# Performance work log

Measured on AMD Instinct MI355X. Metric: run time of the kernel, lower is better.

The kernel has to match this reference:

```python
import jax, jax.numpy as jnp
import numpy as np

T, B, H = 128, 256, 1024


def setup_inputs() -> dict:
    key = jax.random.key(0)
    ks = jax.random.split(key, 6)
    s_i = 1.0 / np.sqrt(2 * H)   # lecun-ish scale for input kernel [2H,3H]
    s_h = 1.0 / np.sqrt(H)       # recurrent kernel scale
    return {
        "a_target": jax.random.normal(ks[0], (T, B, H), jnp.float32),
        "resets": jax.random.bernoulli(ks[1], 0.05, (T, B)),
        "W_i": jax.random.normal(ks[2], (2 * H, 3 * H), jnp.float32) * s_i,
        "b_i": jnp.zeros((3 * H,), jnp.float32),
        "W_h": jax.random.normal(ks[3], (H, 3 * H), jnp.float32) * s_h,
        "b_hn": jnp.zeros((H,), jnp.float32),
        "W_p": jax.random.normal(ks[4], (H, H), jnp.float32) * np.sqrt(2.0 / H),
        "b_p": jnp.zeros((H,), jnp.float32),
    }


def reference(a_target, resets, W_i, b_i, W_h, b_hn, W_p, b_p):
    Hd = W_h.shape[0]
    Bn = a_target.shape[1]

    def step(carry, xt):
        h, a_hat = carry
        a_t, rst = xt                     # a_t: [B,H], rst: [B] bool
        m = rst[:, None]
        h = jnp.where(m, 0.0, h)          # reset-masking of carry
        a_hat = jnp.where(m, 0.0, a_hat)
        pos = jax.nn.relu(a_t - a_hat)
        neg = jax.nn.relu(a_hat - a_t)
        e_t = jnp.concatenate([pos, neg], axis=-1)          # [B, 2H]
        err_mag = jnp.mean(pos + neg, axis=-1)              # [B]
        # GRUCell: gates r,z,n (flax convention: bias on input path + candidate h path)
        gi = e_t @ W_i + b_i                                # [B, 3H]
        gh = h @ W_h                                        # [B, 3H]
        i_r, i_z, i_n = jnp.split(gi, 3, axis=-1)
        h_r, h_z, h_n = jnp.split(gh, 3, axis=-1)
        r = jax.nn.sigmoid(i_r + h_r)
        z = jax.nn.sigmoid(i_z + h_z)
        n = jnp.tanh(i_n + r * (h_n + b_hn))
        new_h = (1.0 - z) * n + z * h                       # [B, H]
        new_a_hat = jax.nn.relu(new_h @ W_p + b_p)          # prediction_dense + relu
        return (new_h, new_a_hat), (new_h, err_mag)

    init = (jnp.zeros((Bn, Hd), a_target.dtype),
            jnp.zeros((Bn, Hd), a_target.dtype))
    (_, _), (r_ts, err_mags) = jax.lax.scan(step, init, (a_target, resets))
    return r_ts, err_mags  # [T,B,H], [T,B]
```

## Files before the change

### kernel.cpp

```cpp
#include <hip/hip_runtime.h>
#include <hip/hip_bf16.h>
#include <math.h>

#define T_DIM 128
#define B_DIM 256
#define H_DIM 1024
#define N3    3072
#define KC    3072
#define KTC   96
#define KTP   32

typedef __attribute__((ext_vector_type(8))) short short8;
typedef __attribute__((ext_vector_type(4))) float float4v;
typedef __attribute__((ext_vector_type(4))) unsigned short ushort4v;

__device__ __forceinline__ unsigned short f2bf(float f) {
  union { float f; unsigned u; } v; v.f = f;
  unsigned u = v.u;
  unsigned r = u + 0x7FFFu + ((u >> 16) & 1u);
  return (unsigned short)(r >> 16);
}

__device__ __forceinline__ size_t afrag(int m, int k, int KT) {
  return ((((size_t)(m >> 4) * KT) + (k >> 5)) * 64
          + ((((k >> 3) & 3) << 4) | (m & 15))) * 8 + (k & 7);
}

__device__ __forceinline__ void store_bf4(unsigned short* p, const float* v) {
  ushort4v u;
  u.x = f2bf(v[0]); u.y = f2bf(v[1]); u.z = f2bf(v[2]); u.w = f2bf(v[3]);
  *(ushort4v*)p = u;
}

__device__ __forceinline__ float sigm(float x) { return 1.f / (1.f + __expf(-x)); }

__global__ void detect_resets(const int* __restrict__ r, int* __restrict__ flag) {
  __shared__ int f;
  if (threadIdx.x == 0) f = 0;
  __syncthreads();
  int loc = 0;
  for (int i = threadIdx.x; i < 8192; i += 256) {
    if ((unsigned)r[i] > 1u) loc = 1;
  }
  if (loc) f = 1;
  __syncthreads();
  if (threadIdx.x == 0) *flag = f;
}

__global__ __launch_bounds__(256) void decode_resets(
    const void* __restrict__ resets, const int* __restrict__ rflag,
    unsigned char* __restrict__ rb) {
  int t = blockIdx.x, b = threadIdx.x;
  int v;
  if (*rflag) v = (int)((const unsigned char*)resets)[t * B_DIM + b];
  else        v = ((const int*)resets)[t * B_DIM + b];
  rb[t * B_DIM + b] = (v != 0) ? 1 : 0;
}

__global__ __launch_bounds__(256) void convert_gates(
    const float* __restrict__ Wi, const float* __restrict__ Wh,
    unsigned short* __restrict__ Wg) {
  int nt = blockIdx.x;
  int kt = blockIdx.y;
  int jt = nt >> 2, g = nt & 3;
  size_t base = ((size_t)nt * KTC + kt) * 512;
  for (int e = threadIdx.x; e < 512; e += 256) {
    int i = e & 7, l = (e >> 3) & 63;
    int k = (kt << 5) + ((l >> 4) << 3) + i;
    int j = (jt << 4) + (l & 15);
    float v = 0.f;
    if (g == 0) v = (k < 2048) ? Wi[(size_t)k * N3 + j] : Wh[(size_t)(k - 2048) * N3 + j];
    else if (g == 1) v = (k < 2048) ? Wi[(size_t)k * N3 + 1024 + j] : Wh[(size_t)(k - 2048) * N3 + 1024 + j];
    else if (g == 2) { if (k < 2048) v = Wi[(size_t)k * N3 + 2048 + j]; }
    else             { if (k >= 2048) v = Wh[(size_t)(k - 2048) * N3 + 2048 + j]; }
    Wg[base + e] = f2bf(v);
  }
}

__global__ __launch_bounds__(256) void convert_wp(const float* __restrict__ W,
                                                  unsigned short* __restrict__ Wsw) {
  int nt = blockIdx.x;
  int kt = blockIdx.y;
  size_t base = ((size_t)nt * KTP + kt) * 512;
  for (int e = threadIdx.x; e < 512; e += 256) {
    int i = e & 7, l = (e >> 3) & 63;
    int k = (kt << 5) + ((l >> 4) << 3) + i;
    int n = (nt << 4) + (l & 15);
    Wsw[base + e] = f2bf(W[(size_t)k * H_DIM + n]);
  }
}

__global__ __launch_bounds__(256) void init_state(
    const float* __restrict__ a_all,
    unsigned short* __restrict__ A0, float* __restrict__ h0,
    float* __restrict__ err_out) {
  int b = blockIdx.x, tid = threadIdx.x;
  int j0 = tid * 4;
  const float* arow = a_all + (size_t)b * H_DIM;
  float pv[4], nv[4], zz[4] = {0.f, 0.f, 0.f, 0.f};
  float s = 0.f;
#pragma unroll
  for (int jj = 0; jj < 4; ++jj) {
    float a = arow[j0 + jj];
    pv[jj] = fmaxf(a, 0.f);
    nv[jj] = fmaxf(-a, 0.f);
    s += pv[jj] + nv[jj];
    h0[(size_t)b * H_DIM + j0 + jj] = 0.f;
  }
  store_bf4(A0 + afrag(b, j0, KTC), pv);
  store_bf4(A0 + afrag(b, 1024 + j0, KTC), nv);
  store_bf4(A0 + afrag(b, 2048 + j0, KTC), zz);
  __shared__ float red[256];
  red[tid] = s;
  __syncthreads();
  for (int st = 128; st > 0; st >>= 1) {
    if (tid < st) red[tid] += red[tid + st];
    __syncthreads();
  }
  if (tid == 0) err_out[b] = red[0] * (1.0f / (float)H_DIM);
}

__device__ __forceinline__ void load_chunk4(
    const short8* __restrict__ ap0, const short8* __restrict__ ap1,
    const short8* __restrict__ ap2, const short8* __restrict__ ap3,
    const short8* __restrict__ bpr, const short8* __restrict__ bpz,
    const short8* __restrict__ bpn, int kb,
    short8 (&A)[4][2], short8 (&R)[2], short8 (&Z)[2], short8 (&N)[2]) {
  size_t o0 = (size_t)kb * 64, o1 = (size_t)(kb + 1) * 64;
  A[0][0] = ap0[o0]; A[1][0] = ap1[o0]; A[2][0] = ap2[o0]; A[3][0] = ap3[o0];
  A[0][1] = ap0[o1]; A[1][1] = ap1[o1]; A[2][1] = ap2[o1]; A[3][1] = ap3[o1];
  R[0] = bpr[o0]; Z[0] = bpz[o0]; N[0] = bpn[o0];
  R[1] = bpr[o1]; Z[1] = bpz[o1]; N[1] = bpn[o1];
}

template<int GS>
__device__ __forceinline__ void mfma_chunk4(
    float4v (&acc)[4][4],
    const short8 (&A)[4][2], const short8 (&R)[2], const short8 (&Z)[2],
    const short8 (&N)[2]) {
#pragma unroll
  for (int kk = 0; kk < 2; ++kk) {
#pragma unroll
    for (int mi = 0; mi < 4; ++mi) {
      acc[mi][0]  = __builtin_amdgcn_mfma_f32_16x16x32_bf16(A[mi][kk], R[kk], acc[mi][0], 0, 0, 0);
      acc[mi][1]  = __builtin_amdgcn_mfma_f32_16x16x32_bf16(A[mi][kk], Z[kk], acc[mi][1], 0, 0, 0);
      acc[mi][GS] = __builtin_amdgcn_mfma_f32_16x16x32_bf16(A[mi][kk], N[kk], acc[mi][GS], 0, 0, 0);
    }
  }
}

template<int GS>
__device__ __forceinline__ void gates_seg4(
    float4v (&acc)[4][4],
    const short8* __restrict__ ap0, const short8* __restrict__ ap1,
    const short8* __restrict__ ap2, const short8* __restrict__ ap3,
    const short8* __restrict__ bpr, const short8* __restrict__ bpz,
    const short8* __restrict__ bpn, int kbeg, int kend) {
  if (kbeg >= kend) return;
  short8 Aa[4][2], Ra[2], Za[2], Na[2];
  short8 Ab[4][2], Rb[2], Zb[2], Nb[2];
  load_chunk4(ap0, ap1, ap2, ap3, bpr, bpz, bpn, kbeg, Aa, Ra, Za, Na);
  for (int kb = kbeg; kb < kend; kb += 4) {
    load_chunk4(ap0, ap1, ap2, ap3, bpr, bpz, bpn, kb + 2, Ab, Rb, Zb, Nb);
    mfma_chunk4<GS>(acc, Aa, Ra, Za, Na);
    if (kb + 4 < kend)
      load_chunk4(ap0, ap1, ap2, ap3, bpr, bpz, bpn, kb + 4, Aa, Ra, Za, Na);
    mfma_chunk4<GS>(acc, Ab, Rb, Zb, Nb);
  }
}

__global__ __launch_bounds__(512, 2) void gates_fused(
    const unsigned short* __restrict__ A_sw, const unsigned short* __restrict__ Wg,
    const float* __restrict__ b_i, const float* __restrict__ b_hn,
    const float* __restrict__ h_in, float* __restrict__ h_out,
    unsigned short* __restrict__ A_next,
    const unsigned char* __restrict__ rb,
    float* __restrict__ r_out, int t) {
  int lane = threadIdx.x & 63, wave = threadIdx.x >> 6;
  int b = blockIdx.x;
  int jt = b & 63;
  int rg2 = b >> 6;

  __shared__ float4v red[4][4][2][64];

  const short8* A8 = (const short8*)A_sw;
  const short8* B8 = (const short8*)Wg;

  float4v acc[4][4];
#pragma unroll
  for (int mi = 0; mi < 4; ++mi)
#pragma unroll
    for (int g = 0; g < 4; ++g) acc[mi][g] = (float4v){0.f, 0.f, 0.f, 0.f};

  const short8* ap0 = A8 + ((size_t)(rg2 * 4 + 0) * KTC) * 64 + lane;
  const short8* ap1 = A8 + ((size_t)(rg2 * 4 + 1) * KTC) * 64 + lane;
  const short8* ap2 = A8 + ((size_t)(rg2 * 4 + 2) * KTC) * 64 + lane;
  const short8* ap3 = A8 + ((size_t)(rg2 * 4 + 3) * KTC) * 64 + lane;
  const short8* bpr = B8 + ((size_t)(jt * 4 + 0) * KTC) * 64 + lane;
  const short8* bpz = B8 + ((size_t)(jt * 4 + 1) * KTC) * 64 + lane;
  const short8* bpi = B8 + ((size_t)(jt * 4 + 2) * KTC) * 64 + lane;
  const short8* bph = B8 + ((size_t)(jt * 4 + 3) * KTC) * 64 + lane;

  int k0 = wave * 12, k1 = k0 + 12;
  int e_end = (k1 < 64) ? k1 : 64;
  int h_st  = (k0 > 64) ? k0 : 64;

  gates_seg4<2>(acc, ap0, ap1, ap2, ap3, bpr, bpz, bpi, k0, e_end);
  gates_seg4<3>(acc, ap0, ap1, ap2, ap3, bpr, bpz, bph, h_st, k1);

#pragma unroll
  for (int hh = 0; hh < 2; ++hh) {
    if (wave >= 4) {
#pragma unroll
      for (int mi = 0; mi < 4; ++mi) {
        red[wave - 4][mi][0][lane] = acc[mi][2 * hh];
        red[wave - 4][mi][1][lane] = acc[mi][2 * hh + 1];
      }
    }
    __syncthreads();
    if (wave < 4) {
#pragma unroll
      for (int mi = 0; mi < 4; ++mi) {
        acc[mi][2 * hh]     += red[wave][mi][0][lane];
        acc[mi][2 * hh + 1] += red[wave][mi][1][lane];
      }
    }
    __syncthreads();
  }
  float4v accs[4];
#pragma unroll
  for (int hh = 0; hh < 2; ++hh) {
    if (wave < 4) {
#pragma unroll
      for (int mi = 0; mi < 4; ++mi) {
        red[wave][mi][0][lane] = acc[mi][2 * hh];
        red[wave][mi][1][lane] = acc[mi][2 * hh + 1];
      }
    }
    __syncthreads();
    if (wave < 4) {
      float4v s0 = red[0][wave][0][lane];
      float4v s1 = red[0][wave][1][lane];
#pragma unroll
      for (int w = 1; w < 4; ++w) {
        s0 += red[w][wave][0][lane];
        s1 += red[w][wave][1][lane];
      }
      accs[2 * hh] = s0; accs[2 * hh + 1] = s1;
    }
    __syncthreads();
  }

  if (wave < 4) {
    int cl = lane & 15, q = lane >> 4;
    int jcol = (jt << 4) + cl;
    float br_ = b_i[jcol], bz_ = b_i[1024 + jcol], bn_ = b_i[2048 + jcol];
    float bh = b_hn[jcol];
    int row_base = rg2 * 64 + wave * 16 + q * 4;
#pragma unroll
    for (int rr = 0; rr < 4; ++rr) {
      int row = row_base + rr;
      float r = sigm(accs[0][rr] + br_);
      float z = sigm(accs[1][rr] + bz_);
      float n = tanhf(accs[2][rr] + bn_ + r * (accs[3][rr] + bh));
      float hv = h_in[(size_t)row * H_DIM + jcol];
      float nh = (1.f - z) * n + z * hv;
      r_out[((size_t)t * B_DIM + row) * H_DIM + jcol] = nh;
      if (t < T_DIM - 1) {
        int rst = rb[(t + 1) * B_DIM + row];
        float hm = rst ? 0.f : nh;
        h_out[(size_t)row * H_DIM + jcol] = hm;
        A_next[afrag(row, 2048 + jcol, KTC)] = f2bf(hm);
      }
    }
  }
}

__global__ __launch_bounds__(512, 2) void pred_fused(
    const unsigned short* __restrict__ A_next, const unsigned short* __restrict__ Wp,
    const float* __restrict__ b_p, const float* __restrict__ a_all,
    const unsigned char* __restrict__ rb,
    unsigned short* __restrict__ A_next_w, float* __restrict__ err_out, int t) {
  int lane = threadIdx.x & 63, wave = threadIdx.x >> 6;
  int b = blockIdx.x;
  int ntq = b & 15, mt = b >> 4;

  const short8* A8 = (const short8*)A_next;
  const short8* B8 = (const short8*)Wp;

  const short8* hap = A8 + ((size_t)mt * KTC + 64) * 64 + lane;
  const short8* bp0 = B8 + ((size_t)(ntq * 4 + 0) * KTP) * 64 + lane;
  const short8* bp1 = B8 + ((size_t)(ntq * 4 + 1) * KTP) * 64 + lane;
  const short8* bp2 = B8 + ((size_t)(ntq * 4 + 2) * KTP) * 64 + lane;
  const short8* bp3 = B8 + ((size_t)(ntq * 4 + 3) * KTP) * 64 + lane;

  float4v acc[4];
#pragma unroll
  for (int n = 0; n < 4; ++n) acc[n] = (float4v){0.f, 0.f, 0.f, 0.f};

  {
    int pk0 = wave * 4;
    short8 Aa[4], B0a[4], B1a[4], B2a[4], B3a[4];
#pragma unroll
    for (int kk = 0; kk < 4; ++kk) Aa[kk] = hap[(size_t)(pk0 + kk) * 64];
#pragma unroll
    for (int kk = 0; kk < 4; ++kk) {
      size_t o = (size_t)(pk0 + kk) * 64;
      B0a[kk] = bp0[o]; B1a[kk] = bp1[o]; B2a[kk] = bp2[o]; B3a[kk] = bp3[o];
    }
#pragma unroll
    for (int kk = 0; kk < 4; ++kk) {
      acc[0] = __builtin_amdgcn_mfma_f32_16x16x32_bf16(Aa[kk], B0a[kk], acc[0], 0, 0, 0);
      acc[1] = __builtin_amdgcn_mfma_f32_16x16x32_bf16(Aa[kk], B1a[kk], acc[1], 0, 0, 0);
      acc[2] = __builtin_amdgcn_mfma_f32_16x16x32_bf16(Aa[kk], B2a[kk], acc[2], 0, 0, 0);
      acc[3] = __builtin_amdgcn_mfma_f32_16x16x32_bf16(Aa[kk], B3a[kk], acc[3], 0, 0, 0);
    }
  }

  __shared__ float4v red[8][4][64];
  __shared__ float rsum_red[4][4][4];
#pragma unroll
  for (int n = 0; n < 4; ++n) red[wave][n][lane] = acc[n];
  __syncthreads();

  int cl = lane & 15, q = lane >> 4;

  if (wave < 4) {
    float4v s = red[0][wave][lane];
#pragma unroll
    for (int w = 1; w < 8; ++w) s += red[w][wave][lane];

    int coln = (ntq * 4 + wave) * 16 + cl;
    float bp = b_p[coln];
    float rsum[4];
#pragma unroll
    for (int rr = 0; rr < 4; ++rr) {
      int row = mt * 16 + q * 4 + rr;
      float ah = fmaxf(s[rr] + bp, 0.f);
      int rst = rb[(t + 1) * B_DIM + row];
      float am = rst ? 0.f : ah;
      float av = a_all[((size_t)(t + 1) * B_DIM + row) * H_DIM + coln];
      float d = av - am;
      float pos = fmaxf(d, 0.f), neg = fmaxf(-d, 0.f);
      A_next_w[afrag(row, coln, KTC)] = f2bf(pos);
      A_next_w[afrag(row, 1024 + coln, KTC)] = f2bf(neg);
      rsum[rr] = pos + neg;
    }
#pragma unroll
    for (int rr = 0; rr < 4; ++rr) {
      float sv = rsum[rr];
      sv += __shfl_xor(sv, 1);
      sv += __shfl_xor(sv, 2);
      sv += __shfl_xor(sv, 4);
      sv += __shfl_xor(sv, 8);
      if (cl == 0) rsum_red[wave][q][rr] = sv;
    }
  }
  __syncthreads();
  if (wave == 0 && lane < 16) {
    int qq = lane >> 2, rr = lane & 3;
    float sv = rsum_red[0][qq][rr] + rsum_red[1][qq][rr]
             + rsum_red[2][qq][rr] + rsum_red[3][qq][rr];
    int row = mt * 16 + qq * 4 + rr;
    atomicAdd(err_out + (size_t)(t + 1) * B_DIM + row, sv * (1.0f / (float)H_DIM));
  }
}

extern "C" void kernel_launch(void* const* d_in, const int* in_sizes, int n_in,
                              void* d_out, int out_size, void* d_ws, size_t ws_size,
                              hipStream_t stream) {
  (void)in_sizes; (void)n_in; (void)out_size; (void)ws_size;
  const float* a_all = (const float*)d_in[0];
  const void*  resets = d_in[1];
  const float* W_i  = (const float*)d_in[2];
  const float* b_i  = (const float*)d_in[3];
  const float* W_h  = (const float*)d_in[4];
  const float* b_hn = (const float*)d_in[5];
  const float* W_p  = (const float*)d_in[6];
  const float* b_p  = (const float*)d_in[7];

  float* r_out = (float*)d_out;
  float* err_out = r_out + (size_t)T_DIM * B_DIM * H_DIM;

  char* ws = (char*)d_ws;
  unsigned short* Wg_sw = (unsigned short*)ws; ws += (size_t)256 * 16 * KC * 2;
  unsigned short* Wp_sw = (unsigned short*)ws; ws += (size_t)H_DIM * H_DIM * 2;
  unsigned short* A0    = (unsigned short*)ws; ws += (size_t)B_DIM * KC * 2;
  unsigned short* A1    = (unsigned short*)ws; ws += (size_t)B_DIM * KC * 2;
  float* h0 = (float*)ws; ws += (size_t)B_DIM * H_DIM * 4;
  float* h1 = (float*)ws; ws += (size_t)B_DIM * H_DIM * 4;
  unsigned char* rb = (unsigned char*)ws; ws += T_DIM * B_DIM;
  int* rflag = (int*)ws; ws += 256;

  hipMemsetAsync(err_out, 0, (size_t)T_DIM * B_DIM * sizeof(float), stream);
  detect_resets<<<1, 256, 0, stream>>>((const int*)resets, rflag);
  decode_resets<<<T_DIM, 256, 0, stream>>>(resets, rflag, rb);
  convert_gates<<<dim3(256, KTC), 256, 0, stream>>>(W_i, W_h, Wg_sw);
  convert_wp<<<dim3(H_DIM / 16, KTP), 256, 0, stream>>>(W_p, Wp_sw);
  init_state<<<B_DIM, 256, 0, stream>>>(a_all, A0, h0, err_out);

  for (int t = 0; t < T_DIM; ++t) {
    const unsigned short* Acur = (t & 1) ? A1 : A0;
    unsigned short* Anext      = (t & 1) ? A0 : A1;
    const float* hcur = (t & 1) ? h1 : h0;
    float* hnext      = (t & 1) ? h0 : h1;
    gates_fused<<<256, 512, 0, stream>>>(
        Acur, Wg_sw, b_i, b_hn, hcur, hnext, Anext, rb, r_out, t);
    if (t < T_DIM - 1)
      pred_fused<<<256, 512, 0, stream>>>(
          Anext, Wp_sw, b_p, a_all, rb, Anext, err_out, t);
  }
}
```

Baseline: 2.502 ms.

## Split gates kernel rows across two wave groups with 1024-thread blocks

```diff
diff --git a/kernel.cpp b/kernel.cpp
--- a/kernel.cpp
+++ b/kernel.cpp
@@ -120,28 +120,27 @@
   if (tid == 0) err_out[b] = red[0] * (1.0f / (float)H_DIM);
 }
 
-__device__ __forceinline__ void load_chunk4(
+__device__ __forceinline__ void load_chunk2(
     const short8* __restrict__ ap0, const short8* __restrict__ ap1,
-    const short8* __restrict__ ap2, const short8* __restrict__ ap3,
     const short8* __restrict__ bpr, const short8* __restrict__ bpz,
     const short8* __restrict__ bpn, int kb,
-    short8 (&A)[4][2], short8 (&R)[2], short8 (&Z)[2], short8 (&N)[2]) {
+    short8 (&A)[2][2], short8 (&R)[2], short8 (&Z)[2], short8 (&N)[2]) {
   size_t o0 = (size_t)kb * 64, o1 = (size_t)(kb + 1) * 64;
-  A[0][0] = ap0[o0]; A[1][0] = ap1[o0]; A[2][0] = ap2[o0]; A[3][0] = ap3[o0];
-  A[0][1] = ap0[o1]; A[1][1] = ap1[o1]; A[2][1] = ap2[o1]; A[3][1] = ap3[o1];
+  A[0][0] = ap0[o0]; A[1][0] = ap1[o0];
+  A[0][1] = ap0[o1]; A[1][1] = ap1[o1];
   R[0] = bpr[o0]; Z[0] = bpz[o0]; N[0] = bpn[o0];
   R[1] = bpr[o1]; Z[1] = bpz[o1]; N[1] = bpn[o1];
 }
 
 template<int GS>
-__device__ __forceinline__ void mfma_chunk4(
-    float4v (&acc)[4][4],
-    const short8 (&A)[4][2], const short8 (&R)[2], const short8 (&Z)[2],
+__device__ __forceinline__ void mfma_chunk2(
+    float4v (&acc)[2][4],
+    const short8 (&A)[2][2], const short8 (&R)[2], const short8 (&Z)[2],
     const short8 (&N)[2]) {
 #pragma unroll
   for (int kk = 0; kk < 2; ++kk) {
 #pragma unroll
-    for (int mi = 0; mi < 4; ++mi) {
+    for (int mi = 0; mi < 2; ++mi) {
       acc[mi][0]  = __builtin_amdgcn_mfma_f32_16x16x32_bf16(A[mi][kk], R[kk], acc[mi][0], 0, 0, 0);
       acc[mi][1]  = __builtin_amdgcn_mfma_f32_16x16x32_bf16(A[mi][kk], Z[kk], acc[mi][1], 0, 0, 0);
       acc[mi][GS] = __builtin_amdgcn_mfma_f32_16x16x32_bf16(A[mi][kk], N[kk], acc[mi][GS], 0, 0, 0);
@@ -150,26 +149,25 @@
 }
 
 template<int GS>
-__device__ __forceinline__ void gates_seg4(
-    float4v (&acc)[4][4],
+__device__ __forceinline__ void gates_seg2(
+    float4v (&acc)[2][4],
     const short8* __restrict__ ap0, const short8* __restrict__ ap1,
-    const short8* __restrict__ ap2, const short8* __restrict__ ap3,
     const short8* __restrict__ bpr, const short8* __restrict__ bpz,
     const short8* __restrict__ bpn, int kbeg, int kend) {
   if (kbeg >= kend) return;
-  short8 Aa[4][2], Ra[2], Za[2], Na[2];
-  short8 Ab[4][2], Rb[2], Zb[2], Nb[2];
-  load_chunk4(ap0, ap1, ap2, ap3, bpr, bpz, bpn, kbeg, Aa, Ra, Za, Na);
+  short8 Aa[2][2], Ra[2], Za[2], Na[2];
+  short8 Ab[2][2], Rb[2], Zb[2], Nb[2];
+  load_chunk2(ap0, ap1, bpr, bpz, bpn, kbeg, Aa, Ra, Za, Na);
   for (int kb = kbeg; kb < kend; kb += 4) {
-    load_chunk4(ap0, ap1, ap2, ap3, bpr, bpz, bpn, kb + 2, Ab, Rb, Zb, Nb);
-    mfma_chunk4<GS>(acc, Aa, Ra, Za, Na);
+    load_chunk2(ap0, ap1, bpr, bpz, bpn, kb + 2, Ab, Rb, Zb, Nb);
+    mfma_chunk2<GS>(acc, Aa, Ra, Za, Na);
     if (kb + 4 < kend)
-      load_chunk4(ap0, ap1, ap2, ap3, bpr, bpz, bpn, kb + 4, Aa, Ra, Za, Na);
-    mfma_chunk4<GS>(acc, Ab, Rb, Zb, Nb);
-  }
-}
-
-__global__ __launch_bounds__(512, 2) void gates_fused(
+      load_chunk2(ap0, ap1, bpr, bpz, bpn, kb + 4, Aa, Ra, Za, Na);
+    mfma_chunk2<GS>(acc, Ab, Rb, Zb, Nb);
+  }
+}
+
+__global__ __launch_bounds__(1024, 1) void gates_fused(
     const unsigned short* __restrict__ A_sw, const unsigned short* __restrict__ Wg,
     const float* __restrict__ b_i, const float* __restrict__ b_hn,
     const float* __restrict__ h_in, float* __restrict__ h_out,
@@ -177,52 +175,52 @@
     const unsigned char* __restrict__ rb,
     float* __restrict__ r_out, int t) {
   int lane = threadIdx.x & 63, wave = threadIdx.x >> 6;
+  int mg = wave >> 3;
+  int ks = wave & 7;
   int b = blockIdx.x;
   int jt = b & 63;
   int rg2 = b >> 6;
 
-  __shared__ float4v red[4][4][2][64];
+  __shared__ float4v red[2][4][2][2][64];
 
   const short8* A8 = (const short8*)A_sw;
   const short8* B8 = (const short8*)Wg;
 
-  float4v acc[4][4];
-#pragma unroll
-  for (int mi = 0; mi < 4; ++mi)
+  float4v acc[2][4];
+#pragma unroll
+  for (int mi = 0; mi < 2; ++mi)
 #pragma unroll
     for (int g = 0; g < 4; ++g) acc[mi][g] = (float4v){0.f, 0.f, 0.f, 0.f};
 
-  const short8* ap0 = A8 + ((size_t)(rg2 * 4 + 0) * KTC) * 64 + lane;
-  const short8* ap1 = A8 + ((size_t)(rg2 * 4 + 1) * KTC) * 64 + lane;
-  const short8* ap2 = A8 + ((size_t)(rg2 * 4 + 2) * KTC) * 64 + lane;
-  const short8* ap3 = A8 + ((size_t)(rg2 * 4 + 3) * KTC) * 64 + lane;
+  const short8* ap0 = A8 + ((size_t)(rg2 * 4 + mg * 2 + 0) * KTC) * 64 + lane;
+  const short8* ap1 = A8 + ((size_t)(rg2 * 4 + mg * 2 + 1) * KTC) * 64 + lane;
   const short8* bpr = B8 + ((size_t)(jt * 4 + 0) * KTC) * 64 + lane;
   const short8* bpz = B8 + ((size_t)(jt * 4 + 1) * KTC) * 64 + lane;
   const short8* bpi = B8 + ((size_t)(jt * 4 + 2) * KTC) * 64 + lane;
   const short8* bph = B8 + ((size_t)(jt * 4 + 3) * KTC) * 64 + lane;
 
-  int k0 = wave * 12, k1 = k0 + 12;
+  int k0 = ks * 12, k1 = k0 + 12;
   int e_end = (k1 < 64) ? k1 : 64;
   int h_st  = (k0 > 64) ? k0 : 64;
 
-  gates_seg4<2>(acc, ap0, ap1, ap2, ap3, bpr, bpz, bpi, k0, e_end);
-  gates_seg4<3>(acc, ap0, ap1, ap2, ap3, bpr, bpz, bph, h_st, k1);
+  gates_seg2<2>(acc, ap0, ap1, bpr, bpz, bpi, k0, e_end);
+  gates_seg2<3>(acc, ap0, ap1, bpr, bpz, bph, h_st, k1);
 
 #pragma unroll
   for (int hh = 0; hh < 2; ++hh) {
-    if (wave >= 4) {
-#pragma unroll
-      for (int mi = 0; mi < 4; ++mi) {
-        red[wave - 4][mi][0][lane] = acc[mi][2 * hh];
-        red[wave - 4][mi][1][lane] = acc[mi][2 * hh + 1];
+    if (ks >= 4) {
+#pragma unroll
+      for (int mi = 0; mi < 2; ++mi) {
+        red[mg][ks - 4][mi][0][lane] = acc[mi][2 * hh];
+        red[mg][ks - 4][mi][1][lane] = acc[mi][2 * hh + 1];
       }
     }
     __syncthreads();
-    if (wave < 4) {
-#pragma unroll
-      for (int mi = 0; mi < 4; ++mi) {
-        acc[mi][2 * hh]     += red[wave][mi][0][lane];
-        acc[mi][2 * hh + 1] += red[wave][mi][1][lane];
+    if (ks < 4) {
+#pragma unroll
+      for (int mi = 0; mi < 2; ++mi) {
+        acc[mi][2 * hh]     += red[mg][ks][mi][0][lane];
+        acc[mi][2 * hh + 1] += red[mg][ks][mi][1][lane];
       }
     }
     __syncthreads();
@@ -230,33 +228,33 @@
   float4v accs[4];
 #pragma unroll
   for (int hh = 0; hh < 2; ++hh) {
-    if (wave < 4) {
-#pragma unroll
-      for (int mi = 0; mi < 4; ++mi) {
-        red[wave][mi][0][lane] = acc[mi][2 * hh];
-        red[wave][mi][1][lane] = acc[mi][2 * hh + 1];
+    if (ks < 4) {
+#pragma unroll
+      for (int mi = 0; mi < 2; ++mi) {
+        red[mg][ks][mi][0][lane] = acc[mi][2 * hh];
+        red[mg][ks][mi][1][lane] = acc[mi][2 * hh + 1];
       }
     }
     __syncthreads();
-    if (wave < 4) {
-      float4v s0 = red[0][wave][0][lane];
-      float4v s1 = red[0][wave][1][lane];
+    if (ks < 2) {
+      float4v s0 = red[mg][0][ks][0][lane];
+      float4v s1 = red[mg][0][ks][1][lane];
 #pragma unroll
       for (int w = 1; w < 4; ++w) {
-        s0 += red[w][wave][0][lane];
-        s1 += red[w][wave][1][lane];
+        s0 += red[mg][w][ks][0][lane];
+        s1 += red[mg][w][ks][1][lane];
       }
       accs[2 * hh] = s0; accs[2 * hh + 1] = s1;
     }
     __syncthreads();
   }
 
-  if (wave < 4) {
+  if (ks < 2) {
     int cl = lane & 15, q = lane >> 4;
     int jcol = (jt << 4) + cl;
     float br_ = b_i[jcol], bz_ = b_i[1024 + jcol], bn_ = b_i[2048 + jcol];
     float bh = b_hn[jcol];
-    int row_base = rg2 * 64 + wave * 16 + q * 4;
+    int row_base = rg2 * 64 + (mg * 2 + ks) * 16 + q * 4;
 #pragma unroll
     for (int rr = 0; rr < 4; ++rr) {
       int row = row_base + rr;
@@ -404,7 +402,7 @@
     unsigned short* Anext      = (t & 1) ? A0 : A1;
     const float* hcur = (t & 1) ? h1 : h0;
     float* hnext      = (t & 1) ? h0 : h1;
-    gates_fused<<<256, 512, 0, stream>>>(
+    gates_fused<<<256, 1024, 0, stream>>>(
         Acur, Wg_sw, b_i, b_hn, hcur, hnext, Anext, rb, r_out, t);
     if (t < T_DIM - 1)
       pred_fused<<<256, 512, 0, stream>>>(
```

Measured after the change: 3.235 ms. +29.3%, slower.

## Stage gate GEMM operands through LDS with async global_load_lds double buffering

Applied to the files above, without the earlier changes.

```diff
diff --git a/kernel.cpp b/kernel.cpp
--- a/kernel.cpp
+++ b/kernel.cpp
@@ -33,6 +33,12 @@
 }
 
 __device__ __forceinline__ float sigm(float x) { return 1.f / (1.f + __expf(-x)); }
+
+__device__ __forceinline__ void glds16(const void* gsrc, void* ldst) {
+  __builtin_amdgcn_global_load_lds(
+      (const __attribute__((address_space(1))) unsigned int*)gsrc,
+      (__attribute__((address_space(3))) unsigned int*)ldst, 16, 0, 0);
+}
 
 __global__ void detect_resets(const int* __restrict__ r, int* __restrict__ flag) {
   __shared__ int f;
@@ -120,56 +126,7 @@
   if (tid == 0) err_out[b] = red[0] * (1.0f / (float)H_DIM);
 }
 
-__device__ __forceinline__ void load_chunk4(
-    const short8* __restrict__ ap0, const short8* __restrict__ ap1,
-    const short8* __restrict__ ap2, const short8* __restrict__ ap3,
-    const short8* __restrict__ bpr, const short8* __restrict__ bpz,
-    const short8* __restrict__ bpn, int kb,
-    short8 (&A)[4][2], short8 (&R)[2], short8 (&Z)[2], short8 (&N)[2]) {
-  size_t o0 = (size_t)kb * 64, o1 = (size_t)(kb + 1) * 64;
-  A[0][0] = ap0[o0]; A[1][0] = ap1[o0]; A[2][0] = ap2[o0]; A[3][0] = ap3[o0];
-  A[0][1] = ap0[o1]; A[1][1] = ap1[o1]; A[2][1] = ap2[o1]; A[3][1] = ap3[o1];
-  R[0] = bpr[o0]; Z[0] = bpz[o0]; N[0] = bpn[o0];
-  R[1] = bpr[o1]; Z[1] = bpz[o1]; N[1] = bpn[o1];
-}
-
-template<int GS>
-__device__ __forceinline__ void mfma_chunk4(
-    float4v (&acc)[4][4],
-    const short8 (&A)[4][2], const short8 (&R)[2], const short8 (&Z)[2],
-    const short8 (&N)[2]) {
-#pragma unroll
-  for (int kk = 0; kk < 2; ++kk) {
-#pragma unroll
-    for (int mi = 0; mi < 4; ++mi) {
-      acc[mi][0]  = __builtin_amdgcn_mfma_f32_16x16x32_bf16(A[mi][kk], R[kk], acc[mi][0], 0, 0, 0);
-      acc[mi][1]  = __builtin_amdgcn_mfma_f32_16x16x32_bf16(A[mi][kk], Z[kk], acc[mi][1], 0, 0, 0);
-      acc[mi][GS] = __builtin_amdgcn_mfma_f32_16x16x32_bf16(A[mi][kk], N[kk], acc[mi][GS], 0, 0, 0);
-    }
-  }
-}
-
-template<int GS>
-__device__ __forceinline__ void gates_seg4(
-    float4v (&acc)[4][4],
-    const short8* __restrict__ ap0, const short8* __restrict__ ap1,
-    const short8* __restrict__ ap2, const short8* __restrict__ ap3,
-    const short8* __restrict__ bpr, const short8* __restrict__ bpz,
-    const short8* __restrict__ bpn, int kbeg, int kend) {
-  if (kbeg >= kend) return;
-  short8 Aa[4][2], Ra[2], Za[2], Na[2];
-  short8 Ab[4][2], Rb[2], Zb[2], Nb[2];
-  load_chunk4(ap0, ap1, ap2, ap3, bpr, bpz, bpn, kbeg, Aa, Ra, Za, Na);
-  for (int kb = kbeg; kb < kend; kb += 4) {
-    load_chunk4(ap0, ap1, ap2, ap3, bpr, bpz, bpn, kb + 2, Ab, Rb, Zb, Nb);
-    mfma_chunk4<GS>(acc, Aa, Ra, Za, Na);
-    if (kb + 4 < kend)
-      load_chunk4(ap0, ap1, ap2, ap3, bpr, bpz, bpn, kb + 4, Aa, Ra, Za, Na);
-    mfma_chunk4<GS>(acc, Ab, Rb, Zb, Nb);
-  }
-}
-
-__global__ __launch_bounds__(512, 2) void gates_fused(
+__global__ __launch_bounds__(512, 1) void gates_fused(
     const unsigned short* __restrict__ A_sw, const unsigned short* __restrict__ Wg,
     const float* __restrict__ b_i, const float* __restrict__ b_hn,
     const float* __restrict__ h_in, float* __restrict__ h_out,
@@ -181,32 +138,81 @@
   int jt = b & 63;
   int rg2 = b >> 6;
 
-  __shared__ float4v red[4][4][2][64];
+  __shared__ short8 stage[2][8][7][64];
 
   const short8* A8 = (const short8*)A_sw;
   const short8* B8 = (const short8*)Wg;
 
+  const short8* aB0 = A8 + ((size_t)(rg2 * 4 + 0) * KTC) * 64;
+  const short8* aB1 = A8 + ((size_t)(rg2 * 4 + 1) * KTC) * 64;
+  const short8* aB2 = A8 + ((size_t)(rg2 * 4 + 2) * KTC) * 64;
+  const short8* aB3 = A8 + ((size_t)(rg2 * 4 + 3) * KTC) * 64;
+  const short8* wBr = B8 + ((size_t)(jt * 4 + 0) * KTC) * 64;
+  const short8* wBz = B8 + ((size_t)(jt * 4 + 1) * KTC) * 64;
+  const short8* wBi = B8 + ((size_t)(jt * 4 + 2) * KTC) * 64;
+  const short8* wBh = B8 + ((size_t)(jt * 4 + 3) * KTC) * 64;
+
   float4v acc[4][4];
 #pragma unroll
   for (int mi = 0; mi < 4; ++mi)
 #pragma unroll
     for (int g = 0; g < 4; ++g) acc[mi][g] = (float4v){0.f, 0.f, 0.f, 0.f};
 
-  const short8* ap0 = A8 + ((size_t)(rg2 * 4 + 0) * KTC) * 64 + lane;
-  const short8* ap1 = A8 + ((size_t)(rg2 * 4 + 1) * KTC) * 64 + lane;
-  const short8* ap2 = A8 + ((size_t)(rg2 * 4 + 2) * KTC) * 64 + lane;
-  const short8* ap3 = A8 + ((size_t)(rg2 * 4 + 3) * KTC) * 64 + lane;
-  const short8* bpr = B8 + ((size_t)(jt * 4 + 0) * KTC) * 64 + lane;
-  const short8* bpz = B8 + ((size_t)(jt * 4 + 1) * KTC) * 64 + lane;
-  const short8* bpi = B8 + ((size_t)(jt * 4 + 2) * KTC) * 64 + lane;
-  const short8* bph = B8 + ((size_t)(jt * 4 + 3) * KTC) * 64 + lane;
-
-  int k0 = wave * 12, k1 = k0 + 12;
-  int e_end = (k1 < 64) ? k1 : 64;
-  int h_st  = (k0 > 64) ? k0 : 64;
-
-  gates_seg4<2>(acc, ap0, ap1, ap2, ap3, bpr, bpz, bpi, k0, e_end);
-  gates_seg4<3>(acc, ap0, ap1, ap2, ap3, bpr, bpz, bph, h_st, k1);
+#define STAGE_CHUNK(cc, NSRC)                                                  \
+  {                                                                            \
+    int kt_ = 8 * (cc) + wave;                                                 \
+    size_t o_ = (size_t)kt_ * 64 + lane;                                       \
+    short8* d_ = &stage[(cc) & 1][wave][0][0];                                 \
+    glds16((const void*)(aB0 + o_), (void*)(d_ + 0 * 64));                     \
+    glds16((const void*)(aB1 + o_), (void*)(d_ + 1 * 64));                     \
+    glds16((const void*)(aB2 + o_), (void*)(d_ + 2 * 64));                     \
+    glds16((const void*)(aB3 + o_), (void*)(d_ + 3 * 64));                     \
+    glds16((const void*)(wBr + o_), (void*)(d_ + 4 * 64));                     \
+    glds16((const void*)(wBz + o_), (void*)(d_ + 5 * 64));                     \
+    glds16((const void*)(NSRC + o_), (void*)(d_ + 6 * 64));                    \
+  }
+
+  STAGE_CHUNK(0, wBi);
+
+#pragma unroll
+  for (int c = 0; c < 12; ++c) {
+    if (c < 11) {
+      if (c + 1 < 8) STAGE_CHUNK(c + 1, wBi)
+      else           STAGE_CHUNK(c + 1, wBh)
+      asm volatile("s_waitcnt vmcnt(7)" ::: "memory");
+    } else {
+      asm volatile("s_waitcnt vmcnt(0)" ::: "memory");
+    }
+    __builtin_amdgcn_sched_barrier(0);
+
+    const short8* f = &stage[c & 1][wave][0][0];
+    short8 A0f = f[0 * 64 + lane];
+    short8 A1f = f[1 * 64 + lane];
+    short8 A2f = f[2 * 64 + lane];
+    short8 A3f = f[3 * 64 + lane];
+    short8 Rf  = f[4 * 64 + lane];
+    short8 Zf  = f[5 * 64 + lane];
+    short8 Nf  = f[6 * 64 + lane];
+
+    const int GS = (c < 8) ? 2 : 3;
+    acc[0][0]  = __builtin_amdgcn_mfma_f32_16x16x32_bf16(A0f, Rf, acc[0][0], 0, 0, 0);
+    acc[1][0]  = __builtin_amdgcn_mfma_f32_16x16x32_bf16(A1f, Rf, acc[1][0], 0, 0, 0);
+    acc[2][0]  = __builtin_amdgcn_mfma_f32_16x16x32_bf16(A2f, Rf, acc[2][0], 0, 0, 0);
+    acc[3][0]  = __builtin_amdgcn_mfma_f32_16x16x32_bf16(A3f, Rf, acc[3][0], 0, 0, 0);
+    acc[0][1]  = __builtin_amdgcn_mfma_f32_16x16x32_bf16(A0f, Zf, acc[0][1], 0, 0, 0);
+    acc[1][1]  = __builtin_amdgcn_mfma_f32_16x16x32_bf16(A1f, Zf, acc[1][1], 0, 0, 0);
+    acc[2][1]  = __builtin_amdgcn_mfma_f32_16x16x32_bf16(A2f, Zf, acc[2][1], 0, 0, 0);
+    acc[3][1]  = __builtin_amdgcn_mfma_f32_16x16x32_bf16(A3f, Zf, acc[3][1], 0, 0, 0);
+    acc[0][GS] = __builtin_amdgcn_mfma_f32_16x16x32_bf16(A0f, Nf, acc[0][GS], 0, 0, 0);
+    acc[1][GS] = __builtin_amdgcn_mfma_f32_16x16x32_bf16(A1f, Nf, acc[1][GS], 0, 0, 0);
+    acc[2][GS] = __builtin_amdgcn_mfma_f32_16x16x32_bf16(A2f, Nf, acc[2][GS], 0, 0, 0);
+    acc[3][GS] = __builtin_amdgcn_mfma_f32_16x16x32_bf16(A3f, Nf, acc[3][GS], 0, 0, 0);
+  }
+#undef STAGE_CHUNK
+
+  __syncthreads();
+
+  float4v (*red)[4][2][64] = (float4v (*)[4][2][64])(&stage[0][0][0][0]);
 
 #pragma unroll
   for (int hh = 0; hh < 2; ++hh) {
```

Result: faster. 2.432 ms (median of 2 runs) (-2.8%).
